# Kernel tuning notes

Hardware: AMD Instinct MI355X
Metric: run time of the kernel (lower is better)

## Reference

```python
import jax, jax.numpy as jnp
import numpy as np
from jax import lax

B = 32768
L = 200          # window_size
K = 5            # conv kernel
CIN = 6
FLAT = L - K + 1  # 196, conv1d valid output length (out channels = 1)


def setup_inputs() -> dict:
    key = jax.random.key(0)
    ks = jax.random.split(key, 9)
    s = lambda *sh: 1.0 / np.sqrt(sh[-1])
    x = jax.random.normal(ks[0], (B, CIN, L), dtype=jnp.float32)
    conv_w = jax.random.normal(ks[1], (1, CIN, K), dtype=jnp.float32) * (1.0 / np.sqrt(CIN * K))
    conv_b = jax.random.normal(ks[2], (1,), dtype=jnp.float32) * 0.1
    w1 = jax.random.normal(ks[3], (FLAT, 50), dtype=jnp.float32) * (1.0 / np.sqrt(FLAT))
    b1 = jax.random.normal(ks[4], (50,), dtype=jnp.float32) * 0.1
    w2 = jax.random.normal(ks[5], (50, 30), dtype=jnp.float32) * (1.0 / np.sqrt(50))
    b2 = jax.random.normal(ks[6], (30,), dtype=jnp.float32) * 0.1
    w3 = jax.random.normal(ks[7], (30, 15), dtype=jnp.float32) * (1.0 / np.sqrt(30))
    b3 = jax.random.normal(ks[8], (15,), dtype=jnp.float32) * 0.1
    return {"x": x, "conv_w": conv_w, "conv_b": conv_b, "w1": w1, "b1": b1,
            "w2": w2, "b2": b2, "w3": w3, "b3": b3}


def reference(x, conv_w, conv_b, w1, b1, w2, b2, w3, b3):
    # conv1d (valid): [B,6,200] -> [B,1,196]
    y = lax.conv_general_dilated(x, conv_w, window_strides=(1,), padding='VALID',
                                 dimension_numbers=('NCH', 'OIH', 'NCH'))
    y = y + conv_b[None, :, None]
    h = y.reshape(x.shape[0], -1)                       # [B,196]
    h = jax.nn.relu(h @ w1 + b1)                        # [B,50]
    h = jax.nn.relu(h @ w2 + b2)                        # [B,30]
    out = h @ w3 + b3                                   # [B,15]
    # Procrustes orthogonalization of the 3x3 block
    R = out[:, :9].reshape(-1, 3, 3)
    U, _, VT = jnp.linalg.svd(R)                        # batched 3x3 SVD
    det = jnp.linalg.det(jnp.matmul(U, VT))             # [B]
    scale = jnp.stack([jnp.ones_like(det), jnp.ones_like(det), det], axis=1)  # diag(1,1,det)
    R_norm = jnp.matmul(U, VT * scale[:, :, None])      # U @ S @ VT
    return jnp.concatenate([R_norm.reshape(-1, 9), out[:, 9:]], axis=1)
```

## Files before the change

### kernel.cpp

```cpp
#include <hip/hip_runtime.h>
#include <math.h>

#define BATCH 32768
#define LW    200
#define CIN   6
#define KSZ   5
#define FLAT  196
#define NH1   50
#define NH2   30
#define NOUT  15
#define TILEW 57
#define NLD   14

__global__ __launch_bounds__(256) void fused_kernel(
    const float* __restrict__ x,
    const float* __restrict__ cw, const float* __restrict__ cb,
    const float* __restrict__ w1, const float* __restrict__ b1,
    const float* __restrict__ w2, const float* __restrict__ b2,
    const float* __restrict__ w3, const float* __restrict__ b3,
    float* __restrict__ out)
{
    __shared__ float xs[4 * 64 * TILEW];

    const int tid  = threadIdx.x;
    const int wv   = __builtin_amdgcn_readfirstlane(tid >> 6);
    const int lane = tid & 63;
    const int b    = blockIdx.x * 64 + lane;
    const int kstart = 49 * wv;
    const int tbase  = 48 * wv;
    const int off    = wv;

    float* tile = xs + wv * (64 * TILEW);

    float w[CIN][KSZ];
#pragma unroll
    for (int c = 0; c < CIN; ++c)
#pragma unroll
        for (int k = 0; k < KSZ; ++k) w[c][k] = cw[c * KSZ + k];
    const float bias = cb[0];

    int goff[NLD];
    int loff[NLD];
#pragma unroll
    for (int u = 0; u < NLD; ++u) {
        int g   = lane + 64 * u;
        int row = g / NLD;
        int c4  = g - row * NLD;
        goff[u] = row * (CIN * LW) + 4 * c4;
        loff[u] = row * TILEW + 4 * c4;
    }
    const float* xw = x + (size_t)blockIdx.x * 64 * (CIN * LW) + tbase;

    float acc[49];
#pragma unroll
    for (int i = 0; i < 49; ++i) acc[i] = bias;

    float4 buf[NLD];
#pragma unroll
    for (int u = 0; u < NLD; ++u)
        buf[u] = *(const float4*)(xw + goff[u]);

#pragma unroll
    for (int ch = 0; ch < CIN; ++ch) {
#pragma unroll
        for (int u = 0; u < NLD; ++u) {
            float* dst = tile + loff[u];
            dst[0] = buf[u].x; dst[1] = buf[u].y; dst[2] = buf[u].z; dst[3] = buf[u].w;
        }
        if (ch + 1 < CIN) {
#pragma unroll
            for (int u = 0; u < NLD; ++u)
                buf[u] = *(const float4*)(xw + (ch + 1) * LW + goff[u]);
        }
        const float* row = tile + lane * TILEW + off;
        float x0 = row[0], x1 = row[1], x2 = row[2], x3 = row[3];
#pragma unroll
        for (int i = 0; i < 49; ++i) {
            float x4v = row[i + 4];
            float a = acc[i];
            a = fmaf(x0, w[ch][0], a);
            a = fmaf(x1, w[ch][1], a);
            a = fmaf(x2, w[ch][2], a);
            a = fmaf(x3, w[ch][3], a);
            a = fmaf(x4v, w[ch][4], a);
            acc[i] = a;
            x0 = x1; x1 = x2; x2 = x3; x3 = x4v;
        }
    }

    float h1p[NH1];
#pragma unroll
    for (int j = 0; j < NH1; ++j) h1p[j] = 0.f;
#pragma unroll
    for (int ii = 0; ii < 49; ++ii) {
        const float* wrow = w1 + (size_t)(kstart + ii) * NH1;
        float c = acc[ii];
#pragma unroll
        for (int j = 0; j < NH1; ++j) h1p[j] = fmaf(c, wrow[j], h1p[j]);
    }

    __syncthreads();
    float* part = xs;
    if (wv != 0) {
#pragma unroll
        for (int j = 0; j < NH1; ++j)
            part[(wv - 1) * (64 * 53) + lane * 53 + j] = h1p[j];
    }
    __syncthreads();
    if (wv != 0) return;

    float h1[NH1];
#pragma unroll
    for (int j = 0; j < NH1; ++j) {
        float s = h1p[j]
                + part[lane * 53 + j]
                + part[64 * 53 + lane * 53 + j]
                + part[2 * 64 * 53 + lane * 53 + j]
                + b1[j];
        h1[j] = fmaxf(s, 0.f);
    }

    float h2[NH2];
#pragma unroll
    for (int j = 0; j < NH2; ++j) h2[j] = b2[j];
#pragma unroll
    for (int k = 0; k < NH1; ++k) {
        float hk = h1[k];
        const float* row = w2 + k * NH2;
#pragma unroll
        for (int j = 0; j < NH2; ++j) h2[j] = fmaf(hk, row[j], h2[j]);
    }
#pragma unroll
    for (int j = 0; j < NH2; ++j) h2[j] = fmaxf(h2[j], 0.f);

    float o[NOUT];
#pragma unroll
    for (int j = 0; j < NOUT; ++j) o[j] = b3[j];
#pragma unroll
    for (int k = 0; k < NH2; ++k) {
        float hk = h2[k];
        const float* row = w3 + k * NOUT;
#pragma unroll
        for (int j = 0; j < NOUT; ++j) o[j] = fmaf(hk, row[j], o[j]);
    }

    {
        float r00 = o[0], r01 = o[1], r02 = o[2];
        float r10 = o[3], r11 = o[4], r12 = o[5];
        float r20 = o[6], r21 = o[7], r22 = o[8];

        float A[4][4], V[4][4];
        A[0][0] = r00 + r11 + r22;
        A[1][1] = r00 - r11 - r22;
        A[2][2] = r11 - r00 - r22;
        A[3][3] = r22 - r00 - r11;
        A[0][1] = A[1][0] = r21 - r12;
        A[0][2] = A[2][0] = r02 - r20;
        A[0][3] = A[3][0] = r10 - r01;
        A[1][2] = A[2][1] = r01 + r10;
        A[1][3] = A[3][1] = r02 + r20;
        A[2][3] = A[3][2] = r12 + r21;
#pragma unroll
        for (int i = 0; i < 4; ++i)
#pragma unroll
            for (int j = 0; j < 4; ++j) V[i][j] = (i == j) ? 1.f : 0.f;

        const int pr[6][2] = {{0,1},{0,2},{0,3},{1,2},{1,3},{2,3}};
        for (int sweep = 0; sweep < 7; ++sweep) {
#pragma unroll
            for (int pi = 0; pi < 6; ++pi) {
                const int p = pr[pi][0], q = pr[pi][1];
                float apq = A[p][q];
                if (fabsf(apq) > 1e-20f) {
                    float theta = (A[q][q] - A[p][p]) / (2.f * apq);
                    float t = copysignf(1.f, theta) / (fabsf(theta) + sqrtf(1.f + theta * theta));
                    float c = rsqrtf(1.f + t * t);
                    float s = t * c;
#pragma unroll
                    for (int k = 0; k < 4; ++k) {
                        float akp = A[k][p], akq = A[k][q];
                        A[k][p] = c * akp - s * akq;
                        A[k][q] = s * akp + c * akq;
                    }
#pragma unroll
                    for (int k = 0; k < 4; ++k) {
                        float apk = A[p][k], aqk = A[q][k];
                        A[p][k] = c * apk - s * aqk;
                        A[q][k] = s * apk + c * aqk;
                    }
#pragma unroll
                    for (int k = 0; k < 4; ++k) {
                        float vkp = V[k][p], vkq = V[k][q];
                        V[k][p] = c * vkp - s * vkq;
                        V[k][q] = s * vkp + c * vkq;
                    }
                }
            }
        }

        int best = 0;
        float bl = A[0][0];
#pragma unroll
        for (int i = 1; i < 4; ++i)
            if (A[i][i] > bl) { bl = A[i][i]; best = i; }

        float vw = V[0][best], vx = V[1][best], vy = V[2][best], vz = V[3][best];
        float inv = rsqrtf(vw * vw + vx * vx + vy * vy + vz * vz);
        vw *= inv; vx *= inv; vy *= inv; vz *= inv;

        float xx = vx * vx, yy = vy * vy, zz = vz * vz;
        float xy = vx * vy, xz = vx * vz, yz = vy * vz;
        float wx = vw * vx, wy = vw * vy, wz = vw * vz;

        float* ob = out + (long)b * NOUT;
        ob[0]  = 1.f - 2.f * (yy + zz);
        ob[1]  = 2.f * (xy - wz);
        ob[2]  = 2.f * (xz + wy);
        ob[3]  = 2.f * (xy + wz);
        ob[4]  = 1.f - 2.f * (xx + zz);
        ob[5]  = 2.f * (yz - wx);
        ob[6]  = 2.f * (xz - wy);
        ob[7]  = 2.f * (yz + wx);
        ob[8]  = 1.f - 2.f * (xx + yy);
        ob[9]  = o[9];
        ob[10] = o[10];
        ob[11] = o[11];
        ob[12] = o[12];
        ob[13] = o[13];
        ob[14] = o[14];
    }
}

extern "C" void kernel_launch(void* const* d_in, const int* in_sizes, int n_in,
                              void* d_out, int out_size, void* d_ws, size_t ws_size,
                              hipStream_t stream) {
    const float* x  = (const float*)d_in[0];
    const float* cw = (const float*)d_in[1];
    const float* cb = (const float*)d_in[2];
    const float* w1 = (const float*)d_in[3];
    const float* b1 = (const float*)d_in[4];
    const float* w2 = (const float*)d_in[5];
    const float* b2 = (const float*)d_in[6];
    const float* w3 = (const float*)d_in[7];
    const float* b3 = (const float*)d_in[8];
    float* outp = (float*)d_out;

    fused_kernel<<<BATCH / 64, 256, 0, stream>>>(x, cw, cb, w1, b1, w2, b2, w3, b3, outp);
}
```

Baseline: 299.6 us.

## Split conv+FC1 across eight waves per block with two-stage partial reduction

Each 64-sample block now uses 512 threads (8 waves) instead of 4. Each wave computes 24 conv outputs (28 for the last wave) and their FC1 partial sums. The partials are reduced in two shared-memory stages before wave 0 runs the MLP tail and the quaternion-based orthogonalization. This halves per-thread conv and FC1 work and register pressure so more waves can hide latency. In exchange it adds an extra reduction round with barriers, more redundant halo loads of x, and a longer serial tail on wave 0 relative to the shortened work phase.

```diff
diff --git a/kernel.cpp b/kernel.cpp
--- a/kernel.cpp
+++ b/kernel.cpp
@@ -9,35 +9,16 @@
 #define NH1   50
 #define NH2   30
 #define NOUT  15
-#define TILEW 57
-#define NLD   14
-
-__global__ __launch_bounds__(256) void fused_kernel(
-    const float* __restrict__ x,
-    const float* __restrict__ cw, const float* __restrict__ cb,
-    const float* __restrict__ w1, const float* __restrict__ b1,
-    const float* __restrict__ w2, const float* __restrict__ b2,
-    const float* __restrict__ w3, const float* __restrict__ b3,
-    float* __restrict__ out)
+
+
+template<int NS>
+__device__ __forceinline__ void conv_fc1_slice(
+    const float* __restrict__ xw, float* __restrict__ tile, int lane,
+    const float (&w)[CIN][KSZ], float bias,
+    const float* __restrict__ w1, int kstart, float (&h1p)[NH1])
 {
-    __shared__ float xs[4 * 64 * TILEW];
-
-    const int tid  = threadIdx.x;
-    const int wv   = __builtin_amdgcn_readfirstlane(tid >> 6);
-    const int lane = tid & 63;
-    const int b    = blockIdx.x * 64 + lane;
-    const int kstart = 49 * wv;
-    const int tbase  = 48 * wv;
-    const int off    = wv;
-
-    float* tile = xs + wv * (64 * TILEW);
-
-    float w[CIN][KSZ];
-#pragma unroll
-    for (int c = 0; c < CIN; ++c)
-#pragma unroll
-        for (int k = 0; k < KSZ; ++k) w[c][k] = cw[c * KSZ + k];
-    const float bias = cb[0];
+    constexpr int NLD = (NS + 4) / 4;
+    constexpr int TW  = NS + 5;
 
     int goff[NLD];
     int loff[NLD];
@@ -47,13 +28,12 @@
         int row = g / NLD;
         int c4  = g - row * NLD;
         goff[u] = row * (CIN * LW) + 4 * c4;
-        loff[u] = row * TILEW + 4 * c4;
-    }
-    const float* xw = x + (size_t)blockIdx.x * 64 * (CIN * LW) + tbase;
-
-    float acc[49];
-#pragma unroll
-    for (int i = 0; i < 49; ++i) acc[i] = bias;
+        loff[u] = row * TW + 4 * c4;
+    }
+
+    float acc[NS];
+#pragma unroll
+    for (int i = 0; i < NS; ++i) acc[i] = bias;
 
     float4 buf[NLD];
 #pragma unroll
@@ -72,10 +52,10 @@
             for (int u = 0; u < NLD; ++u)
                 buf[u] = *(const float4*)(xw + (ch + 1) * LW + goff[u]);
         }
-        const float* row = tile + lane * TILEW + off;
+        const float* row = tile + lane * TW;
         float x0 = row[0], x1 = row[1], x2 = row[2], x3 = row[3];
 #pragma unroll
-        for (int i = 0; i < 49; ++i) {
+        for (int i = 0; i < NS; ++i) {
             float x4v = row[i + 4];
             float a = acc[i];
             a = fmaf(x0, w[ch][0], a);
@@ -88,20 +68,66 @@
         }
     }
 
-    float h1p[NH1];
-#pragma unroll
-    for (int j = 0; j < NH1; ++j) h1p[j] = 0.f;
-#pragma unroll
-    for (int ii = 0; ii < 49; ++ii) {
+#pragma unroll
+    for (int ii = 0; ii < NS; ++ii) {
         const float* wrow = w1 + (size_t)(kstart + ii) * NH1;
         float c = acc[ii];
 #pragma unroll
         for (int j = 0; j < NH1; ++j) h1p[j] = fmaf(c, wrow[j], h1p[j]);
     }
+}
+
+__global__ __launch_bounds__(512, 4) void fused_kernel(
+    const float* __restrict__ x,
+    const float* __restrict__ cw, const float* __restrict__ cb,
+    const float* __restrict__ w1, const float* __restrict__ b1,
+    const float* __restrict__ w2, const float* __restrict__ b2,
+    const float* __restrict__ w3, const float* __restrict__ b3,
+    float* __restrict__ out)
+{
+    __shared__ float xs[15104];
+
+    const int tid  = threadIdx.x;
+    const int wv   = __builtin_amdgcn_readfirstlane(tid >> 6);
+    const int lane = tid & 63;
+    const int b    = blockIdx.x * 64 + lane;
+    const int kstart = 24 * wv;
+
+    float* tile = xs + wv * (64 * 29);
+
+    float w[CIN][KSZ];
+#pragma unroll
+    for (int c = 0; c < CIN; ++c)
+#pragma unroll
+        for (int k = 0; k < KSZ; ++k) w[c][k] = cw[c * KSZ + k];
+    const float bias = cb[0];
+
+    const float* xw = x + (size_t)blockIdx.x * 64 * (CIN * LW) + kstart;
+
+    float h1p[NH1];
+#pragma unroll
+    for (int j = 0; j < NH1; ++j) h1p[j] = 0.f;
+
+    if (wv == 7)
+        conv_fc1_slice<28>(xw, tile, lane, w, bias, w1, kstart, h1p);
+    else
+        conv_fc1_slice<24>(xw, tile, lane, w, bias, w1, kstart, h1p);
 
     __syncthreads();
     float* part = xs;
-    if (wv != 0) {
+    if (wv >= 4) {
+#pragma unroll
+        for (int j = 0; j < NH1; ++j)
+            part[(wv - 4) * (64 * 53) + lane * 53 + j] = h1p[j];
+    }
+    __syncthreads();
+    if (wv < 4) {
+#pragma unroll
+        for (int j = 0; j < NH1; ++j)
+            h1p[j] += part[wv * (64 * 53) + lane * 53 + j];
+    }
+    __syncthreads();
+    if (wv >= 1 && wv < 4) {
 #pragma unroll
         for (int j = 0; j < NH1; ++j)
             part[(wv - 1) * (64 * 53) + lane * 53 + j] = h1p[j];
@@ -245,5 +271,5 @@
     const float* b3 = (const float*)d_in[8];
     float* outp = (float*)d_out;
 
-    fused_kernel<<<BATCH / 64, 256, 0, stream>>>(x, cw, cb, w1, b1, w2, b2, w3, b3, outp);
+    fused_kernel<<<BATCH / 64, 512, 0, stream>>>(x, cw, cb, w1, b1, w2, b2, w3, b3, outp);
 }
```

Result: slower. 327.1 us (+9.2%).
